# Optimization experiments

Hardware: AMD Instinct MI355X
Metric: run time of the kernel (lower is better)

## Reference

```python
import jax, jax.numpy as jnp
import numpy as np

N, E, H, C = 50000, 800000, 4, 32   # nodes, edges, heads, per-head channels
EMB = 64                              # embedding_dim
VOCAB = 1000                          # input_dim (label vocab)


def _gat_layer(x, src, dst, W, a_src, a_dst, b):
    """PyG GATConv (concat heads, negative_slope=0.2, self-loops already in src/dst)."""
    n = x.shape[0]
    h = (x @ W).reshape(n, H, -1)                 # [N,H,C]
    al_s = (h * a_src).sum(-1)                    # [N,H]
    al_d = (h * a_dst).sum(-1)                    # [N,H]
    e = jax.nn.leaky_relu(al_s[src] + al_d[dst], 0.2)   # [E',H]
    m = jax.ops.segment_max(e, dst, num_segments=n)     # segment softmax (stable)
    p = jnp.exp(e - m[dst])
    s = jax.ops.segment_sum(p, dst, num_segments=n)
    alpha = p / (s[dst] + 1e-16)                  # [E',H]
    out = jax.ops.segment_sum(h[src] * alpha[..., None], dst, num_segments=n)
    return out.reshape(n, -1) + b                 # [N,H*C]


def setup_inputs() -> dict:
    key = jax.random.key(0)
    ks = jax.random.split(key, 16)
    def w(k, shape):
        return jax.random.normal(k, shape, jnp.float32) * 0.1
    return dict(
        label=jax.random.randint(ks[0], (N,), 0, VOCAB),
        edge_index=jax.random.randint(ks[1], (2, E), 0, N),
        weight=jax.random.uniform(ks[2], (E,), jnp.float32),
        request_quantity=jax.random.uniform(ks[3], (N,), jnp.float32),
        emb_table=w(ks[4], (VOCAB, EMB)),
        req_W=w(ks[5], (1, EMB)),
        req_b=jnp.zeros((EMB,), jnp.float32),
        W0=w(ks[6], (2 * EMB, H * C)), a_src0=w(ks[7], (H, C)), a_dst0=w(ks[8], (H, C)), b0=jnp.zeros((H * C,), jnp.float32),
        W1=w(ks[9], (H * C, H * C)), a_src1=w(ks[10], (H, C)), a_dst1=w(ks[11], (H, C)), b1=jnp.zeros((H * C,), jnp.float32),
        W2=w(ks[12], (H * C, H * C)), a_src2=w(ks[13], (H, C)), a_dst2=w(ks[14], (H, C)), b2=jnp.zeros((H * C,), jnp.float32),
    )


def reference(label, edge_index, weight, request_quantity, emb_table, req_W, req_b,
              W0, a_src0, a_dst0, b0, W1, a_src1, a_dst1, b1, W2, a_src2, a_dst2, b2):
    del weight  # GATConv(edge_dim=None): edge weights are not used in attention
    x_emb = emb_table[label]                                  # [N,EMB]
    rq = request_quantity
    rq = (rq - rq.mean()) / (rq.std(ddof=1) + 1e-6)           # torch std uses ddof=1
    req = rq[:, None] @ req_W + req_b                         # [N,EMB]
    x = jnp.concatenate([x_emb, req], axis=-1)                # [N,2*EMB]
    # PyG GATConv adds self-loops by default
    loops = jnp.arange(N)
    src = jnp.concatenate([edge_index[0], loops])
    dst = jnp.concatenate([edge_index[1], loops])
    gelu = lambda t: jax.nn.gelu(t, approximate=False)        # torch nn.GELU is exact
    x = gelu(_gat_layer(x, src, dst, W0, a_src0, a_dst0, b0))
    x = gelu(_gat_layer(x, src, dst, W1, a_src1, a_dst1, b1))
    x = gelu(_gat_layer(x, src, dst, W2, a_src2, a_dst2, b2))
    return x
```

## Files before the change

### kernel.cpp

```cpp
#include <hip/hip_runtime.h>
#include <hip/hip_fp16.h>
#include <math.h>

#define NN 50000
#define NE 800000
#define HC 128
#define NHEAD 4
#define EMB 64
#define STATS_BLOCKS 64
#define NB 196
#define HIST_BLOCKS 196

typedef _Float16 f16x8 __attribute__((ext_vector_type(8)));
typedef float f32x4 __attribute__((ext_vector_type(4)));

__device__ __forceinline__ float lrelu(float x) { return x > 0.0f ? x : 0.2f * x; }
__device__ __forceinline__ float gelu_f(float x) {
    return 0.5f * x * (1.0f + erff(x * 0.70710678118654752440f));
}
__device__ __forceinline__ float sel4(float4 v, int h) {
    float r = v.x;
    r = (h == 1) ? v.y : r;
    r = (h == 2) ? v.z : r;
    r = (h == 3) ? v.w : r;
    return r;
}
__device__ __forceinline__ f16x8 cvt8(float4 a, float4 b) {
    f16x8 v;
    v[0] = (_Float16)a.x; v[1] = (_Float16)a.y; v[2] = (_Float16)a.z; v[3] = (_Float16)a.w;
    v[4] = (_Float16)b.x; v[5] = (_Float16)b.y; v[6] = (_Float16)b.z; v[7] = (_Float16)b.w;
    return v;
}

__global__ void stats_hist_kernel(const float* __restrict__ rq, float* __restrict__ stats,
                                  const int* __restrict__ dst, int* __restrict__ bucketCnt) {
    __shared__ float ls[4], ls2[4];
    __shared__ int cnt[NB];
    if (blockIdx.x < STATS_BLOCKS) {
        int i = blockIdx.x * 256 + threadIdx.x;
        float s = 0.f, s2 = 0.f;
        for (; i < NN; i += STATS_BLOCKS * 256) {
            float v = rq[i];
            s += v; s2 += v * v;
        }
        #pragma unroll
        for (int off = 32; off > 0; off >>= 1) {
            s  += __shfl_down(s, off);
            s2 += __shfl_down(s2, off);
        }
        int lane = threadIdx.x & 63, wid = threadIdx.x >> 6;
        if (lane == 0) { ls[wid] = s; ls2[wid] = s2; }
        __syncthreads();
        if (threadIdx.x == 0) {
            atomicAdd(&stats[0], ls[0] + ls[1] + ls[2] + ls[3]);
            atomicAdd(&stats[1], ls2[0] + ls2[1] + ls2[2] + ls2[3]);
        }
    } else {
        int bb = blockIdx.x - STATS_BLOCKS;
        for (int i = threadIdx.x; i < NB; i += 256) cnt[i] = 0;
        __syncthreads();
        int base = bb * 4096;
        #pragma unroll
        for (int it = 0; it < 16; it++) {
            int i = base + it * 256 + threadIdx.x;
            if (i < NE) atomicAdd(&cnt[dst[i] >> 8], 1);
        }
        __syncthreads();
        for (int i = threadIdx.x; i < NB; i += 256)
            if (cnt[i]) atomicAdd(&bucketCnt[i], cnt[i]);
    }
}

__global__ void bucket_scan_kernel(const int* __restrict__ bucketCnt, int* __restrict__ bucketBase,
                                   int* __restrict__ bucketCursor) {
    __shared__ int tmp[256];
    int t = threadIdx.x;
    int v = (t < NB) ? bucketCnt[t] : 0;
    tmp[t] = v;
    __syncthreads();
    #pragma unroll
    for (int off = 1; off < 256; off <<= 1) {
        int add = (t >= off) ? tmp[t - off] : 0;
        __syncthreads();
        tmp[t] += add;
        __syncthreads();
    }
    int excl = tmp[t] - v;
    if (t <= NB) bucketBase[t] = excl;
    if (t < NB) bucketCursor[t] = excl;
}

__global__ void binA_kernel(const int* __restrict__ src, const int* __restrict__ dst,
                            int* __restrict__ bucketCursor, int2* __restrict__ edge_tmp) {
    __shared__ int cnt[NB];
    __shared__ int cur[NB];
    int t = threadIdx.x;
    for (int i = t; i < NB; i += 256) cnt[i] = 0;
    __syncthreads();
    int base = blockIdx.x * 4096;
    int d[16], s[16];
    #pragma unroll
    for (int it = 0; it < 16; it++) {
        int i = base + it * 256 + t;
        bool ok = i < NE;
        d[it] = ok ? dst[i] : -1;
        s[it] = ok ? src[i] : 0;
        if (ok) atomicAdd(&cnt[d[it] >> 8], 1);
    }
    __syncthreads();
    for (int i = t; i < NB; i += 256)
        cur[i] = cnt[i] ? atomicAdd(&bucketCursor[i], cnt[i]) : 0;
    __syncthreads();
    #pragma unroll
    for (int it = 0; it < 16; it++) {
        if (d[it] >= 0) {
            int b = d[it] >> 8;
            int pos = atomicAdd(&cur[b], 1);
            edge_tmp[pos] = make_int2(s[it], d[it] & 255);
        }
    }
}

__global__ void binB_kernel(const int2* __restrict__ edge_tmp, const int* __restrict__ bucketBase,
                            int* __restrict__ row_start, int* __restrict__ src_sorted) {
    __shared__ int ldeg[256];
    __shared__ int lexcl[256];
    __shared__ int lcur[256];
    int b = blockIdx.x, t = threadIdx.x;
    int base = bucketBase[b], endb = bucketBase[b + 1];
    ldeg[t] = 0;
    __syncthreads();
    for (int i = base + t; i < endb; i += 256)
        atomicAdd(&ldeg[edge_tmp[i].y], 1);
    __syncthreads();
    int v = ldeg[t];
    lexcl[t] = v;
    __syncthreads();
    #pragma unroll
    for (int off = 1; off < 256; off <<= 1) {
        int add = (t >= off) ? lexcl[t - off] : 0;
        __syncthreads();
        lexcl[t] += add;
        __syncthreads();
    }
    int excl = lexcl[t] - v;
    int node = b * 256 + t;
    if (node <= NN) row_start[node] = base + excl;
    lcur[t] = excl;
    __syncthreads();
    for (int i = base + t; i < endb; i += 256) {
        int2 e = edge_tmp[i];
        int pos = atomicAdd(&lcur[e.y], 1);
        src_sorted[base + pos] = e.x;
    }
}

template <int L0>
__launch_bounds__(256)
__global__ void gemm_al_kernel(const __half* __restrict__ xh, const float* __restrict__ W,
                               const float* __restrict__ a_src, const float* __restrict__ a_dst,
                               __half* __restrict__ h, float* __restrict__ als,
                               float* __restrict__ ald,
                               const int* __restrict__ label, const float* __restrict__ rq,
                               const float* __restrict__ emb, const float* __restrict__ reqW,
                               const float* __restrict__ reqb, const float* __restrict__ stats) {
    __shared__ _Float16 sX[64][136];
    __shared__ _Float16 sWt[128][136];
    int t = threadIdx.x;
    int w = t >> 6, l = t & 63;
    int col = l & 15, quad = l >> 4;
    int row0 = blockIdx.x * 64;

    #pragma unroll
    for (int i = 0; i < 16; i++) {
        int idx = t + 256 * i;
        int k = idx >> 5;
        int n4 = (idx & 31) * 4;
        float4 wv = ((const float4*)W)[idx];
        sWt[n4 + 0][k] = (_Float16)wv.x;
        sWt[n4 + 1][k] = (_Float16)wv.y;
        sWt[n4 + 2][k] = (_Float16)wv.z;
        sWt[n4 + 3][k] = (_Float16)wv.w;
    }
    float mean = 0.f, inv = 0.f;
    if (L0) {
        float sum = stats[0], sumsq = stats[1];
        mean = sum / (float)NN;
        float var = (sumsq - sum * sum / (float)NN) / (float)(NN - 1);
        inv = 1.0f / (sqrtf(var) + 1e-6f);
    }
    #pragma unroll
    for (int i = 0; i < 4; i++) {
        int idx = t + 256 * i;
        int r = idx >> 4;
        int q = idx & 15;
        int rr = row0 + r;
        f16x8 v;
        #pragma unroll
        for (int j = 0; j < 8; j++) v[j] = (_Float16)0.f;
        if (rr < NN) {
            if (L0) {
                if (q < 8) {
                    const float4* er = (const float4*)(emb + (size_t)label[rr] * EMB);
                    v = cvt8(er[q * 2], er[q * 2 + 1]);
                } else {
                    int j4 = (q - 8) * 2;
                    float4 w0 = ((const float4*)reqW)[j4],     b0 = ((const float4*)reqb)[j4];
                    float4 w1 = ((const float4*)reqW)[j4 + 1], b1 = ((const float4*)reqb)[j4 + 1];
                    float r2 = (rq[rr] - mean) * inv;
                    v = cvt8(make_float4(r2 * w0.x + b0.x, r2 * w0.y + b0.y,
                                         r2 * w0.z + b0.z, r2 * w0.w + b0.w),
                             make_float4(r2 * w1.x + b1.x, r2 * w1.y + b1.y,
                                         r2 * w1.z + b1.z, r2 * w1.w + b1.w));
                }
            } else {
                v = *(const f16x8*)(xh + (size_t)rr * 128 + q * 8);
            }
        }
        *(f16x8*)&sX[r][q * 8] = v;
    }
    __syncthreads();

    f32x4 zero = {0.f, 0.f, 0.f, 0.f};
    f32x4 acc[8];
    #pragma unroll
    for (int nt = 0; nt < 8; nt++) acc[nt] = zero;
    f16x8 afr[4];
    #pragma unroll
    for (int ks = 0; ks < 4; ks++)
        afr[ks] = *(const f16x8*)&sX[w * 16 + col][ks * 32 + quad * 8];
    #pragma unroll
    for (int nt = 0; nt < 8; nt++) {
        #pragma unroll
        for (int ks = 0; ks < 4; ks++) {
            f16x8 bfr = *(const f16x8*)&sWt[nt * 16 + col][ks * 32 + quad * 8];
            acc[nt] = __builtin_amdgcn_mfma_f32_16x16x32_f16(afr[ks], bfr, acc[nt], 0, 0, 0);
        }
    }

    #pragma unroll
    for (int nt = 0; nt < 8; nt++)
        #pragma unroll
        for (int r = 0; r < 4; r++)
            sX[w * 16 + quad * 4 + r][nt * 16 + col] = (_Float16)acc[nt][r];
    __builtin_amdgcn_wave_barrier();
    #pragma unroll
    for (int i = 0; i < 4; i++) {
        int u = l + 64 * i;
        int r = u >> 4, off = (u & 15) * 8;
        int rr = row0 + w * 16 + r;
        f16x8 v = *(const f16x8*)&sX[w * 16 + r][off];
        if (rr < NN) *(f16x8*)(h + (size_t)rr * 128 + off) = v;
    }

    float as[8], ad[8];
    #pragma unroll
    for (int nt = 0; nt < 8; nt++) {
        as[nt] = a_src[nt * 16 + col];
        ad[nt] = a_dst[nt * 16 + col];
    }
    #pragma unroll
    for (int r = 0; r < 4; r++) {
        float ps[4], pd[4];
        #pragma unroll
        for (int hd = 0; hd < 4; hd++) {
            ps[hd] = acc[2 * hd][r] * as[2 * hd] + acc[2 * hd + 1][r] * as[2 * hd + 1];
            pd[hd] = acc[2 * hd][r] * ad[2 * hd] + acc[2 * hd + 1][r] * ad[2 * hd + 1];
            ps[hd] += __shfl_xor(ps[hd], 1); pd[hd] += __shfl_xor(pd[hd], 1);
            ps[hd] += __shfl_xor(ps[hd], 2); pd[hd] += __shfl_xor(pd[hd], 2);
            ps[hd] += __shfl_xor(ps[hd], 4); pd[hd] += __shfl_xor(pd[hd], 4);
            ps[hd] += __shfl_xor(ps[hd], 8); pd[hd] += __shfl_xor(pd[hd], 8);
        }
        int rr = row0 + w * 16 + quad * 4 + r;
        if (col == 0 && rr < NN) {
            *(float4*)(als + (size_t)rr * 4) = make_float4(ps[0], ps[1], ps[2], ps[3]);
            *(float4*)(ald + (size_t)rr * 4) = make_float4(pd[0], pd[1], pd[2], pd[3]);
        }
    }
}

template <int FINAL>
__launch_bounds__(256)
__global__ void agg_kernel(const __half* __restrict__ h, const float* __restrict__ als_,
                           const float* __restrict__ ald_, const int* __restrict__ row_start,
                           const int* __restrict__ src_sorted, const float* __restrict__ bias,
                           float* __restrict__ outf, __half* __restrict__ outh) {
    __shared__ float lds_p[4][4][68];
    __shared__ int   lds_s[4][64];
    int wid = threadIdx.x >> 6;
    int lane = threadIdx.x & 63;
    int node = blockIdx.x * 4 + wid;
    if (node >= NN) return;
    int sub  = lane >> 4;
    int cg   = lane & 15;
    int c0   = cg * 8;
    int head = cg >> 2;

    int start = row_start[node], end = row_start[node + 1];
    float4 adv = *(const float4*)(ald_ + (size_t)node * 4);
    float4 avs = *(const float4*)(als_ + (size_t)node * 4);

    float p_self = __expf(lrelu(sel4(avs, head) + sel4(adv, head)));
    float pinit = (sub == 0) ? p_self : 0.f;
    float s_sum = pinit;
    float acc[8];
    {
        float4 raw = *(const float4*)(h + (size_t)node * 128 + c0);
        const __half2* q2 = (const __half2*)&raw;
        #pragma unroll
        for (int i = 0; i < 4; i++) {
            float2 f = __half22float2(q2[i]);
            acc[2 * i] = f.x * pinit;
            acc[2 * i + 1] = f.y * pinit;
        }
    }

    for (int base = start; base < end; base += 64) {
        int j = base + lane;
        int my = 0;
        float4 p4 = make_float4(0.f, 0.f, 0.f, 0.f);
        if (j < end) {
            my = src_sorted[j];
            float4 av = *(const float4*)(als_ + (size_t)my * 4);
            p4.x = __expf(lrelu(av.x + adv.x));
            p4.y = __expf(lrelu(av.y + adv.y));
            p4.z = __expf(lrelu(av.z + adv.z));
            p4.w = __expf(lrelu(av.w + adv.w));
        }
        lds_s[wid][lane] = my;
        lds_p[wid][0][lane] = p4.x;
        lds_p[wid][1][lane] = p4.y;
        lds_p[wid][2][lane] = p4.z;
        lds_p[wid][3][lane] = p4.w;
        __builtin_amdgcn_wave_barrier();

        int cnt = end - base;
        if (cnt > 64) cnt = 64;
        for (int jj = 0; jj < cnt; jj += 16) {
            int   s[4];
            float p[4];
            #pragma unroll
            for (int i = 0; i < 4; i++) {
                int e = jj + 4 * i + sub;
                bool v = e < cnt;
                int ec = v ? e : 0;
                s[i] = lds_s[wid][ec];
                float pv = lds_p[wid][head][ec];
                p[i] = v ? pv : 0.f;
            }
            float4 raw[4];
            #pragma unroll
            for (int i = 0; i < 4; i++)
                raw[i] = *(const float4*)(h + (size_t)s[i] * 128 + c0);
            #pragma unroll
            for (int i = 0; i < 4; i++) {
                const __half2* q2 = (const __half2*)&raw[i];
                float2 f0 = __half22float2(q2[0]);
                float2 f1 = __half22float2(q2[1]);
                float2 f2 = __half22float2(q2[2]);
                float2 f3 = __half22float2(q2[3]);
                s_sum += p[i];
                acc[0] += f0.x * p[i]; acc[1] += f0.y * p[i];
                acc[2] += f1.x * p[i]; acc[3] += f1.y * p[i];
                acc[4] += f2.x * p[i]; acc[5] += f2.y * p[i];
                acc[6] += f3.x * p[i]; acc[7] += f3.y * p[i];
            }
        }
        __builtin_amdgcn_wave_barrier();
    }

    #pragma unroll
    for (int i = 0; i < 8; i++) {
        acc[i] += __shfl_xor(acc[i], 16);
        acc[i] += __shfl_xor(acc[i], 32);
    }
    s_sum += __shfl_xor(s_sum, 16);
    s_sum += __shfl_xor(s_sum, 32);

    float invs = 1.0f / (s_sum + 1e-16f);
    float t0 = (sub & 1) ? acc[2] : acc[0];
    float t1 = (sub & 1) ? acc[6] : acc[4];
    float num0 = (sub & 2) ? t1 : t0;
    float u0 = (sub & 1) ? acc[3] : acc[1];
    float u1 = (sub & 1) ? acc[7] : acc[5];
    float num1 = (sub & 2) ? u1 : u0;
    int cc = c0 + 2 * sub;
    float2 bv = *(const float2*)(bias + cc);
    float o0 = gelu_f(num0 * invs + bv.x);
    float o1 = gelu_f(num1 * invs + bv.y);
    if (FINAL) {
        *(float2*)(outf + (size_t)node * 128 + cc) = make_float2(o0, o1);
    } else {
        *(__half2*)(outh + (size_t)node * 128 + cc) = __floats2half2_rn(o0, o1);
    }
}

extern "C" void kernel_launch(void* const* d_in, const int* in_sizes, int n_in,
                              void* d_out, int out_size, void* d_ws, size_t ws_size,
                              hipStream_t stream) {
    const int*   label = (const int*)d_in[0];
    const int*   eidx  = (const int*)d_in[1];
    const float* rq    = (const float*)d_in[3];
    const float* emb   = (const float*)d_in[4];
    const float* reqW  = (const float*)d_in[5];
    const float* reqb  = (const float*)d_in[6];
    const float* W[3]    = {(const float*)d_in[7],  (const float*)d_in[11], (const float*)d_in[15]};
    const float* asrc[3] = {(const float*)d_in[8],  (const float*)d_in[12], (const float*)d_in[16]};
    const float* adst[3] = {(const float*)d_in[9],  (const float*)d_in[13], (const float*)d_in[17]};
    const float* bias[3] = {(const float*)d_in[10], (const float*)d_in[14], (const float*)d_in[18]};

    const int* e_src = eidx;
    const int* e_dst = eidx + NE;

    char* ws = (char*)d_ws;
    size_t off = 0;
    auto A = [&](size_t n) { size_t o = off; off += (n + 255) & ~(size_t)255; return o; };
    size_t o_bcnt  = A(256 * 4);
    size_t o_stats = A(8);
    size_t zero_bytes = off;
    size_t o_bbase = A(257 * 4);
    size_t o_bcur  = A(256 * 4);
    size_t o_row   = A((size_t)(NN + 1) * 4);
    size_t o_etmp  = A((size_t)NE * 8);
    size_t o_srcS  = A((size_t)NE * 4);
    size_t o_x     = A((size_t)NN * 128 * 2);
    size_t o_h     = A((size_t)NN * 128 * 2);
    size_t o_als   = A((size_t)NN * 4 * 4);
    size_t o_ald   = A((size_t)NN * 4 * 4);
    (void)ws_size; (void)n_in; (void)in_sizes; (void)out_size;

    int*    bcnt   = (int*)(ws + o_bcnt);
    float*  stats  = (float*)(ws + o_stats);
    int*    bbase  = (int*)(ws + o_bbase);
    int*    bcur   = (int*)(ws + o_bcur);
    int*    rowst  = (int*)(ws + o_row);
    int2*   etmp   = (int2*)(ws + o_etmp);
    int*    srcS   = (int*)(ws + o_srcS);
    __half* xh     = (__half*)(ws + o_x);
    __half* h      = (__half*)(ws + o_h);
    float*  als    = (float*)(ws + o_als);
    float*  ald    = (float*)(ws + o_ald);

    (void)hipMemsetAsync(ws, 0, zero_bytes, stream);

    stats_hist_kernel<<<STATS_BLOCKS + HIST_BLOCKS, 256, 0, stream>>>(rq, stats, e_dst, bcnt);
    bucket_scan_kernel<<<1, 256, 0, stream>>>(bcnt, bbase, bcur);
    binA_kernel<<<HIST_BLOCKS, 256, 0, stream>>>(e_src, e_dst, bcur, etmp);
    binB_kernel<<<NB, 256, 0, stream>>>(etmp, bbase, rowst, srcS);

    const int gemm_blocks = (NN + 63) / 64;
    const int agg_blocks = (NN + 3) / 4;
    for (int l = 0; l < 3; l++) {
        if (l == 0)
            gemm_al_kernel<1><<<gemm_blocks, 256, 0, stream>>>(xh, W[l], asrc[l], adst[l], h, als, ald,
                                                               label, rq, emb, reqW, reqb, stats);
        else
            gemm_al_kernel<0><<<gemm_blocks, 256, 0, stream>>>(xh, W[l], asrc[l], adst[l], h, als, ald,
                                                               label, rq, emb, reqW, reqb, stats);
        if (l == 2)
            agg_kernel<1><<<agg_blocks, 256, 0, stream>>>(h, als, ald, rowst, srcS, bias[l],
                                                          (float*)d_out, nullptr);
        else
            agg_kernel<0><<<agg_blocks, 256, 0, stream>>>(h, als, ald, rowst, srcS, bias[l],
                                                          nullptr, xh);
    }
}
```

Baseline: 323.4 us.

## Pre-transpose weights to fp16, fold bucket scan into binning kernels, shrink GEMM smem

Weight transposition and fp16 conversion move into a prep kernel that runs once, so each GEMM block copies a ready fp16 transposed tile into shared memory instead of converting fp32 with scattered transposed LDS writes. The single-block bucket scan kernel is removed and every binA and binB block recomputes the 196-entry scan locally, which drops one launch. For layers 1 and 2 the GEMM loads A fragments straight from global memory rather than staging them through shared memory, and uses dynamic shared memory sized per layer, which lowers LDS use and may raise occupancy. The cost is redundant scan work in each block and an extra barrier before the output staging, which now reuses the weight buffer.

```diff
diff --git a/kernel.cpp b/kernel.cpp
--- a/kernel.cpp
+++ b/kernel.cpp
@@ -10,6 +10,8 @@
 #define STATS_BLOCKS 64
 #define NB 196
 #define HIST_BLOCKS 196
+#define WPREP_BLOCKS 192
+#define WT_ROW 136
 
 typedef _Float16 f16x8 __attribute__((ext_vector_type(8)));
 typedef float f32x4 __attribute__((ext_vector_type(4)));
@@ -32,8 +34,10 @@
     return v;
 }
 
-__global__ void stats_hist_kernel(const float* __restrict__ rq, float* __restrict__ stats,
-                                  const int* __restrict__ dst, int* __restrict__ bucketCnt) {
+__global__ void prep_kernel(const float* __restrict__ rq, float* __restrict__ stats,
+                            const int* __restrict__ dst, int* __restrict__ bucketCnt,
+                            const float* __restrict__ W0, const float* __restrict__ W1,
+                            const float* __restrict__ W2, _Float16* __restrict__ wt) {
     __shared__ float ls[4], ls2[4];
     __shared__ int cnt[NB];
     if (blockIdx.x < STATS_BLOCKS) {
@@ -55,7 +59,7 @@
             atomicAdd(&stats[0], ls[0] + ls[1] + ls[2] + ls[3]);
             atomicAdd(&stats[1], ls2[0] + ls2[1] + ls2[2] + ls2[3]);
         }
-    } else {
+    } else if (blockIdx.x < STATS_BLOCKS + HIST_BLOCKS) {
         int bb = blockIdx.x - STATS_BLOCKS;
         for (int i = threadIdx.x; i < NB; i += 256) cnt[i] = 0;
         __syncthreads();
@@ -68,33 +72,44 @@
         __syncthreads();
         for (int i = threadIdx.x; i < NB; i += 256)
             if (cnt[i]) atomicAdd(&bucketCnt[i], cnt[i]);
-    }
-}
-
-__global__ void bucket_scan_kernel(const int* __restrict__ bucketCnt, int* __restrict__ bucketBase,
-                                   int* __restrict__ bucketCursor) {
-    __shared__ int tmp[256];
+    } else {
+        int bb = blockIdx.x - STATS_BLOCKS - HIST_BLOCKS;
+        int l = bb >> 6, blk = bb & 63;
+        const float* W = (l == 0) ? W0 : (l == 1) ? W1 : W2;
+        int idx = blk * 256 + threadIdx.x;
+        int n = idx >> 7, k = idx & 127;
+        wt[(size_t)l * 128 * WT_ROW + n * WT_ROW + k] = (_Float16)W[k * 128 + n];
+    }
+}
+
+__device__ __forceinline__ void scan_buckets(const int* __restrict__ bucketCnt,
+                                             int* sIncl ) {
     int t = threadIdx.x;
     int v = (t < NB) ? bucketCnt[t] : 0;
-    tmp[t] = v;
+    sIncl[t] = v;
     __syncthreads();
     #pragma unroll
     for (int off = 1; off < 256; off <<= 1) {
-        int add = (t >= off) ? tmp[t - off] : 0;
-        __syncthreads();
-        tmp[t] += add;
-        __syncthreads();
-    }
-    int excl = tmp[t] - v;
-    if (t <= NB) bucketBase[t] = excl;
-    if (t < NB) bucketCursor[t] = excl;
+        int add = (t >= off) ? sIncl[t - off] : 0;
+        __syncthreads();
+        sIncl[t] += add;
+        __syncthreads();
+    }
 }
 
 __global__ void binA_kernel(const int* __restrict__ src, const int* __restrict__ dst,
-                            int* __restrict__ bucketCursor, int2* __restrict__ edge_tmp) {
+                            const int* __restrict__ bucketCnt, int* __restrict__ gcur,
+                            int2* __restrict__ edge_tmp) {
+    __shared__ int sIncl[256];
+    __shared__ int sBaseE[256];
     __shared__ int cnt[NB];
     __shared__ int cur[NB];
     int t = threadIdx.x;
+    scan_buckets(bucketCnt, sIncl);
+    {
+        int v = (t < NB) ? bucketCnt[t] : 0;
+        sBaseE[t] = sIncl[t] - v;
+    }
     for (int i = t; i < NB; i += 256) cnt[i] = 0;
     __syncthreads();
     int base = blockIdx.x * 4096;
@@ -109,7 +124,7 @@
     }
     __syncthreads();
     for (int i = t; i < NB; i += 256)
-        cur[i] = cnt[i] ? atomicAdd(&bucketCursor[i], cnt[i]) : 0;
+        cur[i] = cnt[i] ? (sBaseE[i] + atomicAdd(&gcur[i], cnt[i])) : 0;
     __syncthreads();
     #pragma unroll
     for (int it = 0; it < 16; it++) {
@@ -121,15 +136,22 @@
     }
 }
 
-__global__ void binB_kernel(const int2* __restrict__ edge_tmp, const int* __restrict__ bucketBase,
+__global__ void binB_kernel(const int2* __restrict__ edge_tmp, const int* __restrict__ bucketCnt,
                             int* __restrict__ row_start, int* __restrict__ src_sorted) {
+    __shared__ int sIncl[256];
     __shared__ int ldeg[256];
     __shared__ int lexcl[256];
     __shared__ int lcur[256];
+    __shared__ int s_base, s_end;
     int b = blockIdx.x, t = threadIdx.x;
-    int base = bucketBase[b], endb = bucketBase[b + 1];
+    scan_buckets(bucketCnt, sIncl);
+    if (t == 0) {
+        s_end = sIncl[b];
+        s_base = sIncl[b] - bucketCnt[b];
+    }
     ldeg[t] = 0;
     __syncthreads();
+    int base = s_base, endb = s_end;
     for (int i = base + t; i < endb; i += 256)
         atomicAdd(&ldeg[edge_tmp[i].y], 1);
     __syncthreads();
@@ -157,49 +179,45 @@
 
 template <int L0>
 __launch_bounds__(256)
-__global__ void gemm_al_kernel(const __half* __restrict__ xh, const float* __restrict__ W,
+__global__ void gemm_al_kernel(const __half* __restrict__ xh, const _Float16* __restrict__ wt,
                                const float* __restrict__ a_src, const float* __restrict__ a_dst,
                                __half* __restrict__ h, float* __restrict__ als,
                                float* __restrict__ ald,
                                const int* __restrict__ label, const float* __restrict__ rq,
                                const float* __restrict__ emb, const float* __restrict__ reqW,
                                const float* __restrict__ reqb, const float* __restrict__ stats) {
-    __shared__ _Float16 sX[64][136];
-    __shared__ _Float16 sWt[128][136];
+    extern __shared__ char smem[];
+    _Float16* sWt = (_Float16*)smem;
+    _Float16* sX  = sWt + 128 * WT_ROW;
     int t = threadIdx.x;
     int w = t >> 6, l = t & 63;
     int col = l & 15, quad = l >> 4;
     int row0 = blockIdx.x * 64;
 
-    #pragma unroll
-    for (int i = 0; i < 16; i++) {
-        int idx = t + 256 * i;
-        int k = idx >> 5;
-        int n4 = (idx & 31) * 4;
-        float4 wv = ((const float4*)W)[idx];
-        sWt[n4 + 0][k] = (_Float16)wv.x;
-        sWt[n4 + 1][k] = (_Float16)wv.y;
-        sWt[n4 + 2][k] = (_Float16)wv.z;
-        sWt[n4 + 3][k] = (_Float16)wv.w;
-    }
-    float mean = 0.f, inv = 0.f;
+    {
+        const f16x8* g = (const f16x8*)wt;
+        f16x8* s = (f16x8*)sWt;
+        #pragma unroll
+        for (int i = 0; i < 9; i++) {
+            int idx = t + 256 * i;
+            if (idx < 128 * WT_ROW / 8) s[idx] = g[idx];
+        }
+    }
     if (L0) {
         float sum = stats[0], sumsq = stats[1];
-        mean = sum / (float)NN;
+        float mean = sum / (float)NN;
         float var = (sumsq - sum * sum / (float)NN) / (float)(NN - 1);
-        inv = 1.0f / (sqrtf(var) + 1e-6f);
-    }
-    #pragma unroll
-    for (int i = 0; i < 4; i++) {
-        int idx = t + 256 * i;
-        int r = idx >> 4;
-        int q = idx & 15;
-        int rr = row0 + r;
-        f16x8 v;
-        #pragma unroll
-        for (int j = 0; j < 8; j++) v[j] = (_Float16)0.f;
-        if (rr < NN) {
-            if (L0) {
+        float inv = 1.0f / (sqrtf(var) + 1e-6f);
+        #pragma unroll
+        for (int i = 0; i < 4; i++) {
+            int idx = t + 256 * i;
+            int r = idx >> 4;
+            int q = idx & 15;
+            int rr = row0 + r;
+            f16x8 v;
+            #pragma unroll
+            for (int j = 0; j < 8; j++) v[j] = (_Float16)0.f;
+            if (rr < NN) {
                 if (q < 8) {
                     const float4* er = (const float4*)(emb + (size_t)label[rr] * EMB);
                     v = cvt8(er[q * 2], er[q * 2 + 1]);
@@ -213,43 +231,52 @@
                              make_float4(r2 * w1.x + b1.x, r2 * w1.y + b1.y,
                                          r2 * w1.z + b1.z, r2 * w1.w + b1.w));
                 }
-            } else {
-                v = *(const f16x8*)(xh + (size_t)rr * 128 + q * 8);
             }
-        }
-        *(f16x8*)&sX[r][q * 8] = v;
-    }
-    __syncthreads();
+            *(f16x8*)&sX[r * WT_ROW + q * 8] = v;
+        }
+    }
+    __syncthreads();
+
+    f16x8 afr[4];
+    if (L0) {
+        #pragma unroll
+        for (int ks = 0; ks < 4; ks++)
+            afr[ks] = *(const f16x8*)&sX[(w * 16 + col) * WT_ROW + ks * 32 + quad * 8];
+    } else {
+        int rr = row0 + w * 16 + col;
+        const __half* xp = xh + (size_t)rr * 128;
+        #pragma unroll
+        for (int ks = 0; ks < 4; ks++)
+            afr[ks] = *(const f16x8*)(xp + ks * 32 + quad * 8);
+    }
 
     f32x4 zero = {0.f, 0.f, 0.f, 0.f};
     f32x4 acc[8];
     #pragma unroll
     for (int nt = 0; nt < 8; nt++) acc[nt] = zero;
-    f16x8 afr[4];
-    #pragma unroll
-    for (int ks = 0; ks < 4; ks++)
-        afr[ks] = *(const f16x8*)&sX[w * 16 + col][ks * 32 + quad * 8];
     #pragma unroll
     for (int nt = 0; nt < 8; nt++) {
         #pragma unroll
         for (int ks = 0; ks < 4; ks++) {
-            f16x8 bfr = *(const f16x8*)&sWt[nt * 16 + col][ks * 32 + quad * 8];
+            f16x8 bfr = *(const f16x8*)&sWt[(nt * 16 + col) * WT_ROW + ks * 32 + quad * 8];
             acc[nt] = __builtin_amdgcn_mfma_f32_16x16x32_f16(afr[ks], bfr, acc[nt], 0, 0, 0);
         }
     }
-
+    __syncthreads();
+
+    _Float16* sOut = sWt;
     #pragma unroll
     for (int nt = 0; nt < 8; nt++)
         #pragma unroll
         for (int r = 0; r < 4; r++)
-            sX[w * 16 + quad * 4 + r][nt * 16 + col] = (_Float16)acc[nt][r];
+            sOut[(w * 16 + quad * 4 + r) * WT_ROW + nt * 16 + col] = (_Float16)acc[nt][r];
     __builtin_amdgcn_wave_barrier();
     #pragma unroll
     for (int i = 0; i < 4; i++) {
         int u = l + 64 * i;
         int r = u >> 4, off = (u & 15) * 8;
         int rr = row0 + w * 16 + r;
-        f16x8 v = *(const f16x8*)&sX[w * 16 + r][off];
+        f16x8 v = *(const f16x8*)&sOut[(w * 16 + r) * WT_ROW + off];
         if (rr < NN) *(f16x8*)(h + (size_t)rr * 128 + off) = v;
     }
 
@@ -416,47 +443,50 @@
     size_t off = 0;
     auto A = [&](size_t n) { size_t o = off; off += (n + 255) & ~(size_t)255; return o; };
     size_t o_bcnt  = A(256 * 4);
+    size_t o_gcur  = A(256 * 4);
     size_t o_stats = A(8);
     size_t zero_bytes = off;
-    size_t o_bbase = A(257 * 4);
-    size_t o_bcur  = A(256 * 4);
     size_t o_row   = A((size_t)(NN + 1) * 4);
     size_t o_etmp  = A((size_t)NE * 8);
     size_t o_srcS  = A((size_t)NE * 4);
+    size_t o_wt    = A((size_t)3 * 128 * WT_ROW * 2);
     size_t o_x     = A((size_t)NN * 128 * 2);
     size_t o_h     = A((size_t)NN * 128 * 2);
     size_t o_als   = A((size_t)NN * 4 * 4);
     size_t o_ald   = A((size_t)NN * 4 * 4);
     (void)ws_size; (void)n_in; (void)in_sizes; (void)out_size;
 
-    int*    bcnt   = (int*)(ws + o_bcnt);
-    float*  stats  = (float*)(ws + o_stats);
-    int*    bbase  = (int*)(ws + o_bbase);
-    int*    bcur   = (int*)(ws + o_bcur);
-    int*    rowst  = (int*)(ws + o_row);
-    int2*   etmp   = (int2*)(ws + o_etmp);
-    int*    srcS   = (int*)(ws + o_srcS);
-    __half* xh     = (__half*)(ws + o_x);
-    __half* h      = (__half*)(ws + o_h);
-    float*  als    = (float*)(ws + o_als);
-    float*  ald    = (float*)(ws + o_ald);
+    int*      bcnt  = (int*)(ws + o_bcnt);
+    int*      gcur  = (int*)(ws + o_gcur);
+    float*    stats = (float*)(ws + o_stats);
+    int*      rowst = (int*)(ws + o_row);
+    int2*     etmp  = (int2*)(ws + o_etmp);
+    int*      srcS  = (int*)(ws + o_srcS);
+    _Float16* wt    = (_Float16*)(ws + o_wt);
+    __half*   xh    = (__half*)(ws + o_x);
+    __half*   h     = (__half*)(ws + o_h);
+    float*    als   = (float*)(ws + o_als);
+    float*    ald   = (float*)(ws + o_ald);
 
     (void)hipMemsetAsync(ws, 0, zero_bytes, stream);
 
-    stats_hist_kernel<<<STATS_BLOCKS + HIST_BLOCKS, 256, 0, stream>>>(rq, stats, e_dst, bcnt);
-    bucket_scan_kernel<<<1, 256, 0, stream>>>(bcnt, bbase, bcur);
-    binA_kernel<<<HIST_BLOCKS, 256, 0, stream>>>(e_src, e_dst, bcur, etmp);
-    binB_kernel<<<NB, 256, 0, stream>>>(etmp, bbase, rowst, srcS);
+    prep_kernel<<<STATS_BLOCKS + HIST_BLOCKS + WPREP_BLOCKS, 256, 0, stream>>>(
+        rq, stats, e_dst, bcnt, W[0], W[1], W[2], wt);
+    binA_kernel<<<HIST_BLOCKS, 256, 0, stream>>>(e_src, e_dst, bcnt, gcur, etmp);
+    binB_kernel<<<NB, 256, 0, stream>>>(etmp, bcnt, rowst, srcS);
 
     const int gemm_blocks = (NN + 63) / 64;
     const int agg_blocks = (NN + 3) / 4;
+    const int smem_l0 = (128 + 64) * WT_ROW * 2;
+    const int smem_ln = 128 * WT_ROW * 2;
     for (int l = 0; l < 3; l++) {
+        const _Float16* wtl = wt + (size_t)l * 128 * WT_ROW;
         if (l == 0)
-            gemm_al_kernel<1><<<gemm_blocks, 256, 0, stream>>>(xh, W[l], asrc[l], adst[l], h, als, ald,
-                                                               label, rq, emb, reqW, reqb, stats);
+            gemm_al_kernel<1><<<gemm_blocks, 256, smem_l0, stream>>>(
+                xh, wtl, asrc[l], adst[l], h, als, ald, label, rq, emb, reqW, reqb, stats);
         else
-            gemm_al_kernel<0><<<gemm_blocks, 256, 0, stream>>>(xh, W[l], asrc[l], adst[l], h, als, ald,
-                                                               label, rq, emb, reqW, reqb, stats);
+            gemm_al_kernel<0><<<gemm_blocks, 256, smem_ln, stream>>>(
+                xh, wtl, asrc[l], adst[l], h, als, ald, label, rq, emb, reqW, reqb, stats);
         if (l == 2)
             agg_kernel<1><<<agg_blocks, 256, 0, stream>>>(h, als, ald, rowst, srcS, bias[l],
                                                           (float*)d_out, nullptr);
```

Measured after the change: 292.1 us. -9.7%, faster.
